# Kernel tuning notes

Measured on AMD Instinct MI355X. Metric: run time of the kernel, lower is better.

The kernel has to match this reference:

```python
import jax, jax.numpy as jnp
import numpy as np

H = 64; V = 50000; W = 64; N_TD = 8192; L_BU = 4096; N_BU = 2 * L_BU - 1; DEG = 2; NCLASS = 4


def setup_inputs() -> dict:
    rng = np.random.default_rng(0)
    def mat(*s):
        return jnp.asarray(rng.normal(scale=0.1, size=s).astype(np.float32))
    inp = {}
    inp['td_x_word'] = jnp.asarray(rng.random((N_TD, W), dtype=np.float32))
    inp['bu_x_word'] = jnp.asarray(rng.random((N_BU, W), dtype=np.float32))
    for tag in ('td', 'bu'):
        inp['E_' + tag] = mat(H, V)
        for g in ('z', 'r', 'h'):
            inp['W_%s_%s' % (g, tag)] = mat(H, H)
            inp['U_%s_%s' % (g, tag)] = mat(H, H)
            inp['b_%s_%s' % (g, tag)] = jnp.zeros((H,), jnp.float32)
    inp['W_out1'] = mat(H, 2 * H); inp['b_out1'] = jnp.zeros((H,), jnp.float32)
    inp['W_out4'] = mat(NCLASS, H); inp['b_out4'] = jnp.zeros((NCLASS,), jnp.float32)
    inp['td_x_index'] = jnp.asarray(rng.integers(0, V, (N_TD, W)).astype(np.int32))
    inp['bu_x_index'] = jnp.asarray(rng.integers(0, V, (N_BU, W)).astype(np.int32))
    # top-down: node i (stored at node_h row i+1) has parent at node_h row i//2 (row 0 = zero root)
    inp['td_parent'] = jnp.asarray((np.arange(N_TD) // 2).astype(np.int32))
    # leaves = node_h rows never used as a parent: rows (N_TD-1)//2+1 .. N_TD
    inp['td_leaf_idxs'] = jnp.asarray(np.arange((N_TD - 1) // 2 + 1, N_TD + 1).astype(np.int32))
    # bottom-up complete binary tree: leaves 0..L-1, parent j (node L+j) has children 2j, 2j+1
    tree = np.full((L_BU - 1, DEG + 1), -1, np.int32)
    j = np.arange(L_BU - 1)
    tree[:, 0] = 2 * j; tree[:, 1] = 2 * j + 1
    inp['bu_tree'] = jnp.asarray(tree)
    return inp


def _xe(E, idx, word):
    # E:[H,V], idx/word:[N,W] -> per-node embedding [N,H]
    return jnp.einsum('nwh,nw->nh', E.T[idx], word)


def _gru(zx, rx, hx, Uz, Ur, Uh, hprev):
    z = jax.nn.sigmoid(zx + Uz @ hprev)
    r = jax.nn.sigmoid(rx + Ur @ hprev)
    c = jnp.tanh(hx + Uh @ (hprev * r))
    return z * hprev + (1.0 - z) * c


def reference(td_x_word, bu_x_word, E_td, W_z_td, U_z_td, b_z_td, W_r_td, U_r_td, b_r_td,
              W_h_td, U_h_td, b_h_td, E_bu, W_z_bu, U_z_bu, b_z_bu, W_r_bu, U_r_bu, b_r_bu,
              W_h_bu, U_h_bu, b_h_bu, W_out1, b_out1, W_out4, b_out4,
              td_x_index, td_parent, td_leaf_idxs, bu_x_index, bu_tree):
    # ---- top-down tree GRU ----
    xe = _xe(E_td, td_x_index, td_x_word)                    # [N_td, H]
    zx = xe @ W_z_td.T + b_z_td
    rx = xe @ W_r_td.T + b_r_td
    hx = xe @ W_h_td.T + b_h_td
    n, h = xe.shape

    def td_step(node_h, i):
        hnew = _gru(zx[i], rx[i], hx[i], U_z_td, U_r_td, U_h_td, node_h[td_parent[i]])
        return node_h.at[i + 1].set(hnew), None

    node_h, _ = jax.lax.scan(td_step, jnp.zeros((n + 1, h), xe.dtype), jnp.arange(n))
    td_final = node_h[td_leaf_idxs].max(axis=0)              # [H]

    # ---- bottom-up tree GRU ----
    xe_b = _xe(E_bu, bu_x_index, bu_x_word)                  # [N_bu, H]
    zxb = xe_b @ W_z_bu.T + b_z_bu
    rxb = xe_b @ W_r_bu.T + b_r_bu
    hxb = xe_b @ W_h_bu.T + b_h_bu
    n_par = bu_tree.shape[0]
    n_b = xe_b.shape[0]
    L = n_b - n_par
    # leaves: child states are zeros => h_tilde = 0, r irrelevant, h = (1-z)*tanh(hx)
    leaf_h = (1.0 - jax.nn.sigmoid(zxb[:L])) * jnp.tanh(hxb[:L])
    node_hb0 = jnp.zeros((n_b, h), xe_b.dtype).at[:L].set(leaf_h)

    def bu_step(nh, j):
        idx = bu_tree[j, :-1]
        m = (idx > -1).astype(nh.dtype)
        h_tilde = (nh[jnp.clip(idx, 0)] * m[:, None]).sum(axis=0)
        hp = _gru(zxb[L + j], rxb[L + j], hxb[L + j], U_z_bu, U_r_bu, U_h_bu, h_tilde)
        return nh.at[L + j].set(hp), None

    node_hb, _ = jax.lax.scan(bu_step, node_hb0, jnp.arange(n_par))
    bu_root = node_hb[-1]                                    # [H]

    # ---- output head (forward() semantics: ReLU + softmax) ----
    fs = jnp.concatenate([td_final, bu_root])                # [2H]
    fs1 = jax.nn.relu(W_out1 @ fs + b_out1)                  # [H]
    return jax.nn.softmax(W_out4 @ fs1 + b_out4)             # [Nclass]
```

## Files before the change

kernel.cpp:

```cpp
#include <hip/hip_runtime.h>
#include <stdint.h>

typedef unsigned short u16;

#define V 50000
#define NTD 8192
#define NBU 8191

#define ET_TD_OFF   0ul
#define ET_BU_OFF   6400000ul
#define ZRH_TD_OFF  12800000ul
#define ZRH_BU_OFF  19091456ul
#define HBLEAF_OFF  25382144ul
#define TDMAX_OFF   26430720ul
#define BU6_OFF     26447104ul
#define BUROOT_OFF  26463488ul
#define CNT_OFF     26463744ul
#define WS_NEEDED   26464000ul

struct RvParams {
  const void *td_x_word, *bu_x_word;
  const int *td_idx, *bu_idx;
  const void *Wtd[3], *Utd[3], *btd[3];
  const void *Wbu[3], *Ubu[3], *bbu[3];
  const void *W_out1, *b_out1, *W_out4, *b_out4;
  const void *E_td, *E_bu;
  u16 *Et_td, *Et_bu;
  float *zrh_td, *zrh_bu, *hb_leaf, *tdmax, *bu6, *buroot;
  unsigned *cnt;
  void *out;
};

__device__ __forceinline__ float b2f(unsigned u){ return __uint_as_float(u << 16); }
__device__ __forceinline__ u16 f2b(float f){
  unsigned x = __float_as_uint(f);
  unsigned r = x + 0x7fffu + ((x >> 16) & 1u);
  return (u16)(r >> 16);
}
__device__ __forceinline__ float ldq(const void* p, bool f32, size_t i){
  return f32 ? ((const float*)p)[i] : b2f((unsigned)((const u16*)p)[i]);
}
__device__ __forceinline__ float sigm(float x){
  x = fminf(fmaxf(x, -30.f), 30.f);
  return 1.f / (1.f + __expf(-x));
}
__device__ __forceinline__ float tanh_f(float x){
  x = fminf(fmaxf(x, -15.f), 15.f);
  float e = __expf(2.f * x);
  return (e - 1.f) / (e + 1.f);
}
__device__ __forceinline__ float rdlane(float v, int k){
  return __uint_as_float((unsigned)__builtin_amdgcn_readlane((int)__float_as_uint(v), k));
}

__device__ __forceinline__ bool detect_f32_wave(const void* tdw, int lane){
  unsigned u = (unsigned)((const u16*)tdw)[lane];
  unsigned e = (u >> 7) & 0xFFu;
  int bad = ((u >> 15) | (e >= 0x7Fu ? 1u : 0u)) ? 1 : 0;
  unsigned long long m = __ballot(bad);
  return __popcll(m) >= 8;
}

__global__ __launch_bounds__(1024) void k0_transpose(RvParams p){
  const int tx = threadIdx.x & 63, ty = threadIdx.x >> 6;
  const bool f32 = detect_f32_wave(p.td_x_word, tx);
  if (blockIdx.x == 0 && threadIdx.x == 0){ p.cnt[0] = 0u; p.cnt[1] = 0u; }
  __shared__ u16 tile[64][66];
  const int nb = (V + 63) >> 6;
  int b = blockIdx.x;
  const void* src; u16* dst;
  if (b < nb){ src = p.E_td; dst = p.Et_td; }
  else       { src = p.E_bu; dst = p.Et_bu; b -= nb; }
  const int v0 = b << 6;
  #pragma unroll
  for (int i = 0; i < 4; i++){
    int h = ty + (i << 4);
    int v = v0 + tx;
    u16 val = 0;
    if (v < V){
      if (f32) val = f2b(((const float*)src)[(size_t)h * V + v]);
      else     val = ((const u16*)src)[(size_t)h * V + v];
    }
    tile[h][tx] = val;
  }
  __syncthreads();
  #pragma unroll
  for (int i = 0; i < 4; i++){
    int vv = ty + (i << 4);
    int v = v0 + vv;
    if (v < V) dst[(size_t)v * 64 + tx] = tile[tx][vv];
  }
}

__global__ __launch_bounds__(512) void k1_embed(RvParams p){
  const int tid = threadIdx.x, wv = tid >> 6, lane = tid & 63;
  const bool f32 = detect_f32_wave(p.td_x_word, lane);
  __shared__ float sWz[64 * 65], sWr[64 * 65], sWh[64 * 65];
  const bool is_td = blockIdx.x < 1024;
  {
    const void* Wzg = is_td ? p.Wtd[0] : p.Wbu[0];
    const void* Wrg = is_td ? p.Wtd[1] : p.Wbu[1];
    const void* Whg = is_td ? p.Wtd[2] : p.Wbu[2];
    #pragma unroll
    for (int q = 0; q < 8; q++){
      int u = tid + (q << 9);
      int i = u >> 6, k = u & 63;
      sWz[k * 65 + i] = ldq(Wzg, f32, u);
      sWr[k * 65 + i] = ldq(Wrg, f32, u);
      sWh[k * 65 + i] = ldq(Whg, f32, u);
    }
  }
  __syncthreads();
  const int gw = blockIdx.x * 8 + wv;
  int n; const void* xw; const int* xi; const u16* Et;
  if (is_td){ n = gw;        xw = p.td_x_word; xi = p.td_idx; Et = p.Et_td; }
  else      { n = gw - NTD;  xw = p.bu_x_word; xi = p.bu_idx; Et = p.Et_bu; }
  if (!is_td && n >= NBU) return;

  const int   my_idx = xi[(size_t)n * 64 + lane];
  const float my_w   = ldq(xw, f32, (size_t)n * 64 + lane);
  float x0 = 0.f, x1 = 0.f, x2 = 0.f, x3 = 0.f;
  #pragma unroll
  for (int w = 0; w < 64; w += 4){
    int   i0 = __builtin_amdgcn_readlane(my_idx, w);
    int   i1 = __builtin_amdgcn_readlane(my_idx, w + 1);
    int   i2 = __builtin_amdgcn_readlane(my_idx, w + 2);
    int   i3 = __builtin_amdgcn_readlane(my_idx, w + 3);
    x0 = fmaf(rdlane(my_w, w),     b2f((unsigned)Et[(size_t)i0 * 64 + lane]), x0);
    x1 = fmaf(rdlane(my_w, w + 1), b2f((unsigned)Et[(size_t)i1 * 64 + lane]), x1);
    x2 = fmaf(rdlane(my_w, w + 2), b2f((unsigned)Et[(size_t)i2 * 64 + lane]), x2);
    x3 = fmaf(rdlane(my_w, w + 3), b2f((unsigned)Et[(size_t)i3 * 64 + lane]), x3);
  }
  float xe = (x0 + x1) + (x2 + x3);

  float az = ldq(is_td ? p.btd[0] : p.bbu[0], f32, lane);
  float ar = ldq(is_td ? p.btd[1] : p.bbu[1], f32, lane);
  float ah = ldq(is_td ? p.btd[2] : p.bbu[2], f32, lane);
  #pragma unroll
  for (int k = 0; k < 64; k++){
    float xk = rdlane(xe, k);
    az = fmaf(sWz[k * 65 + lane], xk, az);
    ar = fmaf(sWr[k * 65 + lane], xk, ar);
    ah = fmaf(sWh[k * 65 + lane], xk, ah);
  }
  if (is_td){
    float* o = p.zrh_td + (size_t)n * 192;
    o[lane] = az; o[64 + lane] = ar; o[128 + lane] = ah;
  } else if (n < 4096){
    p.hb_leaf[(size_t)n * 64 + lane] = (1.f - sigm(az)) * tanh_f(ah);
  } else {
    float* o = p.zrh_bu + (size_t)n * 192;
    o[lane] = az; o[64 + lane] = ar; o[128 + lane] = ah;
  }
}

template<int NB>
__device__ __forceinline__ void gru_reg(const float (&uz)[64], const float (&ur)[64], const float (&uh)[64],
                                        float (&hp)[NB], const float (&zx)[NB], const float (&rx)[NB],
                                        const float (&hx)[NB], int lane){
  float az[NB], az2[NB], ar[NB], ar2[NB];
  #pragma unroll
  for (int n = 0; n < NB; n++){ az[n] = 0.f; az2[n] = 0.f; ar[n] = 0.f; ar2[n] = 0.f; }
  #pragma unroll
  for (int k = 0; k < 64; k += 2){
    #pragma unroll
    for (int n = 0; n < NB; n++){
      float h0 = rdlane(hp[n], k), h1 = rdlane(hp[n], k + 1);
      az[n]  = fmaf(uz[k],     h0, az[n]);
      az2[n] = fmaf(uz[k + 1], h1, az2[n]);
      ar[n]  = fmaf(ur[k],     h0, ar[n]);
      ar2[n] = fmaf(ur[k + 1], h1, ar2[n]);
    }
  }
  float z[NB], rh[NB];
  #pragma unroll
  for (int n = 0; n < NB; n++){
    z[n]  = sigm(zx[n] + az[n] + az2[n]);
    rh[n] = sigm(rx[n] + ar[n] + ar2[n]) * hp[n];
  }
  float ah[NB], ah2[NB];
  #pragma unroll
  for (int n = 0; n < NB; n++){ ah[n] = 0.f; ah2[n] = 0.f; }
  #pragma unroll
  for (int k = 0; k < 64; k += 2){
    #pragma unroll
    for (int n = 0; n < NB; n++){
      float r0 = rdlane(rh[n], k), r1 = rdlane(rh[n], k + 1);
      ah[n]  = fmaf(uh[k],     r0, ah[n]);
      ah2[n] = fmaf(uh[k + 1], r1, ah2[n]);
    }
  }
  #pragma unroll
  for (int n = 0; n < NB; n++){
    float c = tanh_f(hx[n] + ah[n] + ah2[n]);
    hp[n] = z[n] * hp[n] + (1.f - z[n]) * c;
  }
}

__device__ __forceinline__ void run_level(bool isbu, int cnt, int pbase, int base, int zoff,
                                          const float (&uz)[64], const float (&ur)[64], const float (&uh)[64],
                                          float* hbuf, const float* zbuf, int wv, int lane){
  if (cnt >= 16){
    for (int t0 = wv * 4; t0 < cnt; t0 += 16){
      float hp[4], zx[4], rx[4], hx[4];
      #pragma unroll
      for (int n = 0; n < 4; n++){
        int t = t0 + n;
        hp[n] = isbu ? (hbuf[(pbase + 2 * t) * 64 + lane] + hbuf[(pbase + 2 * t + 1) * 64 + lane])
                     : hbuf[(pbase + (t >> 1)) * 64 + lane];
        const float* zr = zbuf + (size_t)(base + zoff + t) * 192;
        zx[n] = zr[lane]; rx[n] = zr[64 + lane]; hx[n] = zr[128 + lane];
      }
      gru_reg<4>(uz, ur, uh, hp, zx, rx, hx, lane);
      #pragma unroll
      for (int n = 0; n < 4; n++) hbuf[(base + t0 + n) * 64 + lane] = hp[n];
    }
  } else {
    for (int t = wv; t < cnt; t += 4){
      float hp[1], zx[1], rx[1], hx[1];
      hp[0] = isbu ? (hbuf[(pbase + 2 * t) * 64 + lane] + hbuf[(pbase + 2 * t + 1) * 64 + lane])
                   : hbuf[(pbase + (t >> 1)) * 64 + lane];
      const float* zr = zbuf + (size_t)(base + zoff + t) * 192;
      zx[0] = zr[lane]; rx[0] = zr[64 + lane]; hx[0] = zr[128 + lane];
      gru_reg<1>(uz, ur, uh, hp, zx, rx, hx, lane);
      hbuf[(base + t) * 64 + lane] = hp[0];
    }
  }
  __syncthreads();
}

__global__ __launch_bounds__(256, 1) void k2_trees(RvParams p){
  const int tid = threadIdx.x, wv = tid >> 6, lane = tid & 63;
  const bool f32 = detect_f32_wave(p.td_x_word, lane);
  __shared__ __attribute__((aligned(16))) float zbuf[127 * 192];
  __shared__ __attribute__((aligned(16))) float hbuf[127 * 64];
  __shared__ __attribute__((aligned(16))) float scr[4 * 64];
  __shared__ int lastBU, lastAll;
  const bool is_td = blockIdx.x < 64;
  const int  b  = blockIdx.x;
  const int  bb = blockIdx.x - 64;

  float rzv[6], rrv[6], rhv[6], ezv[2], erv[2], ehv[2];
  if (is_td && wv == 0){
    int anc[7]; anc[6] = 63 + b;
    #pragma unroll
    for (int l = 5; l >= 1; l--) anc[l] = (anc[l + 1] - 1) >> 1;
    #pragma unroll
    for (int l = 1; l <= 6; l++){
      const float* zr = p.zrh_td + (size_t)(anc[l] - 1) * 192;
      rzv[l - 1] = zr[lane]; rrv[l - 1] = zr[64 + lane]; rhv[l - 1] = zr[128 + lane];
    }
    if (b == 0){
      #pragma unroll
      for (int n = 0; n < 2; n++){
        const float* zr = p.zrh_td + (size_t)(8190 + n) * 192;
        ezv[n] = zr[lane]; erv[n] = zr[64 + lane]; ehv[n] = zr[128 + lane];
      }
    }
  }

  if (is_td){
    for (int d = 1; d <= 6; d++){
      int cntn = 1 << d;
      size_t pos0 = ((size_t)(64 + b) << d) - 1;
      const float4* g = (const float4*)(p.zrh_td + (pos0 - 1) * 192);
      float4* s = (float4*)(zbuf + (size_t)(cntn - 1) * 192);
      int n4 = cntn * 48;
      for (int i = tid; i < n4; i += 256) s[i] = g[i];
    }
  } else {
    {
      const float4* g = (const float4*)(p.hb_leaf + (size_t)bb * 64 * 64);
      float4* s = (float4*)hbuf;
      for (int i = tid; i < 1024; i += 256) s[i] = g[i];
    }
    for (int l = 1; l <= 6; l++){
      int cntn = 1 << (6 - l);
      int baseC = 128 - (1 << (7 - l));
      {
        int j0 = 4096 - (1 << (13 - l)) + bb * cntn;
        const float4* g = (const float4*)(p.zrh_bu + (size_t)(4096 + j0) * 192);
        float4* s = (float4*)(zbuf + (size_t)baseC * 192);
        int n4 = cntn * 48;
        for (int i = tid; i < n4; i += 256) s[i] = g[i];
      }
      {
        int j0 = 4096 - (1 << (7 - l));
        const float4* g = (const float4*)(p.zrh_bu + (size_t)(4096 + j0) * 192);
        float4* s = (float4*)(zbuf + (size_t)(baseC - 64) * 192);
        int n4 = cntn * 48;
        for (int i = tid; i < n4; i += 256) s[i] = g[i];
      }
    }
  }

  float uz[64], ur[64], uh[64];
  {
    const void* Uzg = is_td ? p.Utd[0] : p.Ubu[0];
    const void* Urg = is_td ? p.Utd[1] : p.Ubu[1];
    const void* Uhg = is_td ? p.Utd[2] : p.Ubu[2];
    if (f32){
      const float4* a = (const float4*)((const float*)Uzg + (size_t)lane * 64);
      const float4* c = (const float4*)((const float*)Urg + (size_t)lane * 64);
      const float4* d = (const float4*)((const float*)Uhg + (size_t)lane * 64);
      #pragma unroll
      for (int q = 0; q < 16; q++){
        float4 vz = a[q], vr = c[q], vh = d[q];
        uz[4*q] = vz.x; uz[4*q+1] = vz.y; uz[4*q+2] = vz.z; uz[4*q+3] = vz.w;
        ur[4*q] = vr.x; ur[4*q+1] = vr.y; ur[4*q+2] = vr.z; ur[4*q+3] = vr.w;
        uh[4*q] = vh.x; uh[4*q+1] = vh.y; uh[4*q+2] = vh.z; uh[4*q+3] = vh.w;
      }
    } else {
      const u16* a = (const u16*)Uzg + (size_t)lane * 64;
      const u16* c = (const u16*)Urg + (size_t)lane * 64;
      const u16* d = (const u16*)Uhg + (size_t)lane * 64;
      #pragma unroll
      for (int k = 0; k < 64; k++){
        uz[k] = b2f((unsigned)a[k]); ur[k] = b2f((unsigned)c[k]); uh[k] = b2f((unsigned)d[k]);
      }
    }
  }
  __syncthreads();

  if (is_td){
    if (wv == 0){
      float hp[1] = {0.f}, zx[1], rx[1], hx[1];
      #pragma unroll
      for (int l = 0; l < 6; l++){
        zx[0] = rzv[l]; rx[0] = rrv[l]; hx[0] = rhv[l];
        gru_reg<1>(uz, ur, uh, hp, zx, rx, hx, lane);
      }
      hbuf[lane] = hp[0];
    }
    __syncthreads();
    for (int d = 1; d <= 6; d++)
      run_level(false, 1 << d, (1 << (d - 1)) - 1, (1 << d) - 1, 0, uz, ur, uh, hbuf, zbuf, wv, lane);
    if (b == 0 && wv == 0){
      float h4095 = hbuf[63 * 64 + lane];
      #pragma unroll
      for (int n = 0; n < 2; n++){
        float hp[1], zx[1], rx[1], hx[1];
        hp[0] = h4095; zx[0] = ezv[n]; rx[0] = erv[n]; hx[0] = ehv[n];
        gru_reg<1>(uz, ur, uh, hp, zx, rx, hx, lane);
        hbuf[(1 + n) * 64 + lane] = hp[0];
      }
    }
    __syncthreads();
    int cl = (b == 0) ? 65 : 64;
    float m = -3.0e38f;
    for (int i = wv; i < cl; i += 4){
      int s;
      if (b == 0) s = (i < 63) ? (64 + i) : ((i == 63) ? 1 : 2);
      else        s = 63 + i;
      m = fmaxf(m, hbuf[s * 64 + lane]);
    }
    scr[wv * 64 + lane] = m;
    __syncthreads();
    if (wv == 0){
      float mm = m;
      #pragma unroll
      for (int w2 = 1; w2 < 4; w2++) mm = fmaxf(mm, scr[w2 * 64 + lane]);
      p.tdmax[b * 64 + lane] = mm;
    }
  } else {
    for (int l = 1; l <= 6; l++)
      run_level(true, 1 << (6 - l), 128 - (1 << (8 - l)), 128 - (1 << (7 - l)), 0, uz, ur, uh, hbuf, zbuf, wv, lane);
    if (wv == 0) p.bu6[bb * 64 + lane] = hbuf[126 * 64 + lane];
    __threadfence();
    if (tid == 0){
      unsigned old = atomicAdd(&p.cnt[0], 1u);
      lastBU = (old == 63u) ? 1 : 0;
    }
    __syncthreads();
    if (lastBU){
      __threadfence();
      {
        const float4* g = (const float4*)p.bu6;
        float4* s = (float4*)hbuf;
        for (int i = tid; i < 1024; i += 256) s[i] = g[i];
      }
      __syncthreads();
      for (int l = 1; l <= 6; l++)
        run_level(true, 1 << (6 - l), 128 - (1 << (8 - l)), 128 - (1 << (7 - l)), -64, uz, ur, uh, hbuf, zbuf, wv, lane);
      if (wv == 0) p.buroot[lane] = hbuf[126 * 64 + lane];
    }
  }

  __threadfence();
  if (tid == 0){
    unsigned old = atomicAdd(&p.cnt[1], 1u);
    lastAll = (old == 127u) ? 1 : 0;
  }
  __syncthreads();
  if (lastAll){
    __threadfence();
    if (wv == 0){
      float m = -3.0e38f;
      #pragma unroll
      for (int bq = 0; bq < 64; bq++) m = fmaxf(m, p.tdmax[bq * 64 + lane]);
      scr[lane] = m;
      scr[64 + lane] = p.buroot[lane];
      __builtin_amdgcn_wave_barrier();
      float a = ldq(p.b_out1, f32, lane);
      for (int j = 0; j < 128; j++) a = fmaf(ldq(p.W_out1, f32, (size_t)lane * 128 + j), scr[j], a);
      scr[128 + lane] = fmaxf(a, 0.f);
      __builtin_amdgcn_wave_barrier();
      if (lane < 4){
        float l = ldq(p.b_out4, f32, lane);
        for (int i = 0; i < 64; i++) l = fmaf(ldq(p.W_out4, f32, (size_t)lane * 64 + i), scr[128 + i], l);
        scr[192 + lane] = l;
      }
      __builtin_amdgcn_wave_barrier();
      if (lane < 4){
        float l0 = scr[192], l1 = scr[193], l2 = scr[194], l3 = scr[195];
        float mx = fmaxf(fmaxf(l0, l1), fmaxf(l2, l3));
        float s = __expf(l0 - mx) + __expf(l1 - mx) + __expf(l2 - mx) + __expf(l3 - mx);
        float prob = __expf(scr[192 + lane] - mx) / s;
        if (f32) ((float*)p.out)[lane] = prob;
        else     ((u16*)p.out)[lane]   = f2b(prob);
      }
    }
  }
}

extern "C" void kernel_launch(void* const* d_in, const int* in_sizes, int n_in,
                              void* d_out, int out_size, void* d_ws, size_t ws_size,
                              hipStream_t stream){
  if (ws_size < WS_NEEDED) return;
  RvParams p;
  p.td_x_word = d_in[0];
  p.bu_x_word = d_in[1];
  p.E_td = d_in[2];
  p.Wtd[0] = d_in[3];  p.Utd[0] = d_in[4];  p.btd[0] = d_in[5];
  p.Wtd[1] = d_in[6];  p.Utd[1] = d_in[7];  p.btd[1] = d_in[8];
  p.Wtd[2] = d_in[9];  p.Utd[2] = d_in[10]; p.btd[2] = d_in[11];
  p.E_bu = d_in[12];
  p.Wbu[0] = d_in[13]; p.Ubu[0] = d_in[14]; p.bbu[0] = d_in[15];
  p.Wbu[1] = d_in[16]; p.Ubu[1] = d_in[17]; p.bbu[1] = d_in[18];
  p.Wbu[2] = d_in[19]; p.Ubu[2] = d_in[20]; p.bbu[2] = d_in[21];
  p.W_out1 = d_in[22]; p.b_out1 = d_in[23];
  p.W_out4 = d_in[24]; p.b_out4 = d_in[25];
  p.td_idx = (const int*)d_in[26];
  const bool dict_order = (in_sizes[27] == NBU * 64);
  p.bu_idx = (const int*)d_in[dict_order ? 27 : 29];

  char* w = (char*)d_ws;
  p.Et_td  = (u16*)  (w + ET_TD_OFF);
  p.Et_bu  = (u16*)  (w + ET_BU_OFF);
  p.zrh_td = (float*)(w + ZRH_TD_OFF);
  p.zrh_bu = (float*)(w + ZRH_BU_OFF);
  p.hb_leaf= (float*)(w + HBLEAF_OFF);
  p.tdmax  = (float*)(w + TDMAX_OFF);
  p.bu6    = (float*)(w + BU6_OFF);
  p.buroot = (float*)(w + BUROOT_OFF);
  p.cnt    = (unsigned*)(w + CNT_OFF);
  p.out    = d_out;

  const int nb = (V + 63) / 64;
  k0_transpose<<<2 * nb, 1024, 0, stream>>>(p);
  k1_embed   <<<2048,    512,  0, stream>>>(p);
  k2_trees   <<<128,     256,  0, stream>>>(p);
}
```

Before: 245.9 us.

## Pack GRU weights as bf16 pairs in registers and restructure embed and tree kernels

Weight matrices are now staged through LDS as packed bf16 pairs and held in 32 registers per gate instead of 64 floats. The embed kernel processes four nodes per wave with register-resident weights across 512 blocks. The tree kernel moves to 512 threads, drops the large LDS zrh staging buffer in favour of per-wave register prefetch of gate inputs, and unrolls each tree level explicitly. The aim is to cut register pressure and LDS traffic, raise per-block parallelism and amortize weight loads. The trade-off is that f32 weights get rounded to bf16, which adds precision loss, and the embed gather now reads index and word values as scalar loads per node.

```diff
diff --git a/kernel.cpp b/kernel.cpp
--- a/kernel.cpp
+++ b/kernel.cpp
@@ -37,6 +37,8 @@
   unsigned r = x + 0x7fffu + ((x >> 16) & 1u);
   return (u16)(r >> 16);
 }
+__device__ __forceinline__ float pklo(unsigned u){ return __uint_as_float(u << 16); }
+__device__ __forceinline__ float pkhi(unsigned u){ return __uint_as_float(u & 0xffff0000u); }
 __device__ __forceinline__ float ldq(const void* p, bool f32, size_t i){
   return f32 ? ((const float*)p)[i] : b2f((unsigned)((const u16*)p)[i]);
 }
@@ -59,6 +61,30 @@
   int bad = ((u >> 15) | (e >= 0x7Fu ? 1u : 0u)) ? 1 : 0;
   unsigned long long m = __ballot(bad);
   return __popcll(m) >= 8;
+}
+
+template<int BT>
+__device__ __forceinline__ void stage_w_packed(unsigned* dst, const void* src, bool f32, int tid){
+  for (int u = tid; u < 2048; u += BT){
+    int q = u & 31, i = u >> 5;
+    unsigned pk;
+    if (f32){
+      float a = ((const float*)src)[i * 64 + 2 * q];
+      float b = ((const float*)src)[i * 64 + 2 * q + 1];
+      pk = (unsigned)f2b(a) | ((unsigned)f2b(b) << 16);
+    } else {
+      pk = ((const unsigned*)src)[i * 32 + q];
+    }
+    dst[q * 65 + i] = pk;
+  }
+}
+__device__ __forceinline__ void load_w_regs(unsigned (&w)[32], const unsigned* lds, int lane){
+  #pragma unroll
+  for (int q = 0; q < 32; q++) w[q] = lds[q * 65 + lane];
+}
+__device__ __forceinline__ void ld3(const float* zrh, size_t idx, float& a, float& b, float& c, int lane){
+  const float* zr = zrh + idx * 192;
+  a = zr[lane]; b = zr[64 + lane]; c = zr[128 + lane];
 }
 
 __global__ __launch_bounds__(1024) void k0_transpose(RvParams p){
@@ -92,84 +118,96 @@
   }
 }
 
-__global__ __launch_bounds__(512) void k1_embed(RvParams p){
+__global__ __launch_bounds__(512, 2) void k1_embed(RvParams p){
   const int tid = threadIdx.x, wv = tid >> 6, lane = tid & 63;
   const bool f32 = detect_f32_wave(p.td_x_word, lane);
-  __shared__ float sWz[64 * 65], sWr[64 * 65], sWh[64 * 65];
-  const bool is_td = blockIdx.x < 1024;
-  {
-    const void* Wzg = is_td ? p.Wtd[0] : p.Wbu[0];
-    const void* Wrg = is_td ? p.Wtd[1] : p.Wbu[1];
-    const void* Whg = is_td ? p.Wtd[2] : p.Wbu[2];
-    #pragma unroll
-    for (int q = 0; q < 8; q++){
-      int u = tid + (q << 9);
-      int i = u >> 6, k = u & 63;
-      sWz[k * 65 + i] = ldq(Wzg, f32, u);
-      sWr[k * 65 + i] = ldq(Wrg, f32, u);
-      sWh[k * 65 + i] = ldq(Whg, f32, u);
-    }
-  }
+  __shared__ unsigned sW0[32 * 65], sW1[32 * 65], sW2[32 * 65];
+  const bool is_td = blockIdx.x < 256;
+  stage_w_packed<512>(sW0, is_td ? p.Wtd[0] : p.Wbu[0], f32, tid);
+  stage_w_packed<512>(sW1, is_td ? p.Wtd[1] : p.Wbu[1], f32, tid);
+  stage_w_packed<512>(sW2, is_td ? p.Wtd[2] : p.Wbu[2], f32, tid);
   __syncthreads();
-  const int gw = blockIdx.x * 8 + wv;
-  int n; const void* xw; const int* xi; const u16* Et;
-  if (is_td){ n = gw;        xw = p.td_x_word; xi = p.td_idx; Et = p.Et_td; }
-  else      { n = gw - NTD;  xw = p.bu_x_word; xi = p.bu_idx; Et = p.Et_bu; }
-  if (!is_td && n >= NBU) return;
-
-  const int   my_idx = xi[(size_t)n * 64 + lane];
-  const float my_w   = ldq(xw, f32, (size_t)n * 64 + lane);
-  float x0 = 0.f, x1 = 0.f, x2 = 0.f, x3 = 0.f;
-  #pragma unroll
-  for (int w = 0; w < 64; w += 4){
-    int   i0 = __builtin_amdgcn_readlane(my_idx, w);
-    int   i1 = __builtin_amdgcn_readlane(my_idx, w + 1);
-    int   i2 = __builtin_amdgcn_readlane(my_idx, w + 2);
-    int   i3 = __builtin_amdgcn_readlane(my_idx, w + 3);
-    x0 = fmaf(rdlane(my_w, w),     b2f((unsigned)Et[(size_t)i0 * 64 + lane]), x0);
-    x1 = fmaf(rdlane(my_w, w + 1), b2f((unsigned)Et[(size_t)i1 * 64 + lane]), x1);
-    x2 = fmaf(rdlane(my_w, w + 2), b2f((unsigned)Et[(size_t)i2 * 64 + lane]), x2);
-    x3 = fmaf(rdlane(my_w, w + 3), b2f((unsigned)Et[(size_t)i3 * 64 + lane]), x3);
-  }
-  float xe = (x0 + x1) + (x2 + x3);
-
-  float az = ldq(is_td ? p.btd[0] : p.bbu[0], f32, lane);
-  float ar = ldq(is_td ? p.btd[1] : p.bbu[1], f32, lane);
-  float ah = ldq(is_td ? p.btd[2] : p.bbu[2], f32, lane);
-  #pragma unroll
-  for (int k = 0; k < 64; k++){
-    float xk = rdlane(xe, k);
-    az = fmaf(sWz[k * 65 + lane], xk, az);
-    ar = fmaf(sWr[k * 65 + lane], xk, ar);
-    ah = fmaf(sWh[k * 65 + lane], xk, ah);
-  }
-  if (is_td){
-    float* o = p.zrh_td + (size_t)n * 192;
-    o[lane] = az; o[64 + lane] = ar; o[128 + lane] = ah;
-  } else if (n < 4096){
-    p.hb_leaf[(size_t)n * 64 + lane] = (1.f - sigm(az)) * tanh_f(ah);
-  } else {
-    float* o = p.zrh_bu + (size_t)n * 192;
-    o[lane] = az; o[64 + lane] = ar; o[128 + lane] = ah;
+  unsigned wz[32], wr[32], wh[32];
+  load_w_regs(wz, sW0, lane);
+  load_w_regs(wr, sW1, lane);
+  load_w_regs(wh, sW2, lane);
+
+  const int fam  = is_td ? blockIdx.x : (blockIdx.x - 256);
+  const int n0   = fam * 32 + wv * 4;
+  const int nmax = is_td ? NTD : NBU;
+  const int*  xi = is_td ? p.td_idx : p.bu_idx;
+  const void* xw = is_td ? p.td_x_word : p.bu_x_word;
+  const u16*  Et = is_td ? p.Et_td : p.Et_bu;
+
+  int nn[4]; bool val[4];
+  #pragma unroll
+  for (int j = 0; j < 4; j++){
+    val[j] = (n0 + j < nmax);
+    nn[j]  = val[j] ? (n0 + j) : (nmax - 1);
+  }
+  float xe[4] = {0.f, 0.f, 0.f, 0.f};
+  #pragma unroll 8
+  for (int w = 0; w < 64; w++){
+    #pragma unroll
+    for (int j = 0; j < 4; j++){
+      int   iw = xi[(size_t)nn[j] * 64 + w];
+      float wd = ldq(xw, f32, (size_t)nn[j] * 64 + w);
+      xe[j] = fmaf(wd, b2f((unsigned)Et[(size_t)iw * 64 + lane]), xe[j]);
+    }
+  }
+  float az[4], az2[4], ar[4], ar2[4], ah[4], ah2[4];
+  #pragma unroll
+  for (int j = 0; j < 4; j++){ az[j]=az2[j]=ar[j]=ar2[j]=ah[j]=ah2[j]=0.f; }
+  #pragma unroll
+  for (int q = 0; q < 32; q++){
+    float z0 = pklo(wz[q]), z1 = pkhi(wz[q]);
+    float r0 = pklo(wr[q]), r1 = pkhi(wr[q]);
+    float g0 = pklo(wh[q]), g1 = pkhi(wh[q]);
+    #pragma unroll
+    for (int j = 0; j < 4; j++){
+      float x0 = rdlane(xe[j], 2 * q), x1 = rdlane(xe[j], 2 * q + 1);
+      az[j] = fmaf(z0, x0, az[j]);  az2[j] = fmaf(z1, x1, az2[j]);
+      ar[j] = fmaf(r0, x0, ar[j]);  ar2[j] = fmaf(r1, x1, ar2[j]);
+      ah[j] = fmaf(g0, x0, ah[j]);  ah2[j] = fmaf(g1, x1, ah2[j]);
+    }
+  }
+  float bz = ldq(is_td ? p.btd[0] : p.bbu[0], f32, lane);
+  float br = ldq(is_td ? p.btd[1] : p.bbu[1], f32, lane);
+  float bh = ldq(is_td ? p.btd[2] : p.bbu[2], f32, lane);
+  #pragma unroll
+  for (int j = 0; j < 4; j++){
+    if (!val[j]) continue;
+    int n = n0 + j;
+    float zxv = bz + az[j] + az2[j];
+    float rxv = br + ar[j] + ar2[j];
+    float hxv = bh + ah[j] + ah2[j];
+    if (is_td){
+      float* o = p.zrh_td + (size_t)n * 192;
+      o[lane] = zxv; o[64 + lane] = rxv; o[128 + lane] = hxv;
+    } else if (n < 4096){
+      p.hb_leaf[(size_t)n * 64 + lane] = (1.f - sigm(zxv)) * tanh_f(hxv);
+    } else {
+      float* o = p.zrh_bu + (size_t)n * 192;
+      o[lane] = zxv; o[64 + lane] = rxv; o[128 + lane] = hxv;
+    }
   }
 }
 
 template<int NB>
-__device__ __forceinline__ void gru_reg(const float (&uz)[64], const float (&ur)[64], const float (&uh)[64],
-                                        float (&hp)[NB], const float (&zx)[NB], const float (&rx)[NB],
-                                        const float (&hx)[NB], int lane){
+__device__ __forceinline__ void gru_pk(const unsigned (&uz)[32], const unsigned (&ur)[32], const unsigned (&uh)[32],
+                                       float (&hp)[NB], const float* zx, const float* rx, const float* hx){
   float az[NB], az2[NB], ar[NB], ar2[NB];
   #pragma unroll
-  for (int n = 0; n < NB; n++){ az[n] = 0.f; az2[n] = 0.f; ar[n] = 0.f; ar2[n] = 0.f; }
-  #pragma unroll
-  for (int k = 0; k < 64; k += 2){
+  for (int n = 0; n < NB; n++){ az[n] = az2[n] = ar[n] = ar2[n] = 0.f; }
+  #pragma unroll
+  for (int q = 0; q < 32; q++){
+    float wz0 = pklo(uz[q]), wz1 = pkhi(uz[q]);
+    float wr0 = pklo(ur[q]), wr1 = pkhi(ur[q]);
     #pragma unroll
     for (int n = 0; n < NB; n++){
-      float h0 = rdlane(hp[n], k), h1 = rdlane(hp[n], k + 1);
-      az[n]  = fmaf(uz[k],     h0, az[n]);
-      az2[n] = fmaf(uz[k + 1], h1, az2[n]);
-      ar[n]  = fmaf(ur[k],     h0, ar[n]);
-      ar2[n] = fmaf(ur[k + 1], h1, ar2[n]);
+      float h0 = rdlane(hp[n], 2 * q), h1 = rdlane(hp[n], 2 * q + 1);
+      az[n] = fmaf(wz0, h0, az[n]);  az2[n] = fmaf(wz1, h1, az2[n]);
+      ar[n] = fmaf(wr0, h0, ar[n]);  ar2[n] = fmaf(wr1, h1, ar2[n]);
     }
   }
   float z[NB], rh[NB];
@@ -180,14 +218,14 @@
   }
   float ah[NB], ah2[NB];
   #pragma unroll
-  for (int n = 0; n < NB; n++){ ah[n] = 0.f; ah2[n] = 0.f; }
-  #pragma unroll
-  for (int k = 0; k < 64; k += 2){
+  for (int n = 0; n < NB; n++){ ah[n] = ah2[n] = 0.f; }
+  #pragma unroll
+  for (int q = 0; q < 32; q++){
+    float wh0 = pklo(uh[q]), wh1 = pkhi(uh[q]);
     #pragma unroll
     for (int n = 0; n < NB; n++){
-      float r0 = rdlane(rh[n], k), r1 = rdlane(rh[n], k + 1);
-      ah[n]  = fmaf(uh[k],     r0, ah[n]);
-      ah2[n] = fmaf(uh[k + 1], r1, ah2[n]);
+      float r0 = rdlane(rh[n], 2 * q), r1 = rdlane(rh[n], 2 * q + 1);
+      ah[n] = fmaf(wh0, r0, ah[n]);  ah2[n] = fmaf(wh1, r1, ah2[n]);
     }
   }
   #pragma unroll
@@ -197,158 +235,131 @@
   }
 }
 
-__device__ __forceinline__ void run_level(bool isbu, int cnt, int pbase, int base, int zoff,
-                                          const float (&uz)[64], const float (&ur)[64], const float (&uh)[64],
-                                          float* hbuf, const float* zbuf, int wv, int lane){
-  if (cnt >= 16){
-    for (int t0 = wv * 4; t0 < cnt; t0 += 16){
-      float hp[4], zx[4], rx[4], hx[4];
-      #pragma unroll
-      for (int n = 0; n < 4; n++){
-        int t = t0 + n;
-        hp[n] = isbu ? (hbuf[(pbase + 2 * t) * 64 + lane] + hbuf[(pbase + 2 * t + 1) * 64 + lane])
-                     : hbuf[(pbase + (t >> 1)) * 64 + lane];
-        const float* zr = zbuf + (size_t)(base + zoff + t) * 192;
-        zx[n] = zr[lane]; rx[n] = zr[64 + lane]; hx[n] = zr[128 + lane];
-      }
-      gru_reg<4>(uz, ur, uh, hp, zx, rx, hx, lane);
-      #pragma unroll
-      for (int n = 0; n < 4; n++) hbuf[(base + t0 + n) * 64 + lane] = hp[n];
-    }
-  } else {
-    for (int t = wv; t < cnt; t += 4){
-      float hp[1], zx[1], rx[1], hx[1];
-      hp[0] = isbu ? (hbuf[(pbase + 2 * t) * 64 + lane] + hbuf[(pbase + 2 * t + 1) * 64 + lane])
-                   : hbuf[(pbase + (t >> 1)) * 64 + lane];
-      const float* zr = zbuf + (size_t)(base + zoff + t) * 192;
-      zx[0] = zr[lane]; rx[0] = zr[64 + lane]; hx[0] = zr[128 + lane];
-      gru_reg<1>(uz, ur, uh, hp, zx, rx, hx, lane);
-      hbuf[(base + t) * 64 + lane] = hp[0];
-    }
-  }
-  __syncthreads();
-}
-
-__global__ __launch_bounds__(256, 1) void k2_trees(RvParams p){
+template<int NB>
+__device__ __forceinline__ void td_nodes(const unsigned (&uz)[32], const unsigned (&ur)[32], const unsigned (&uh)[32],
+                                         float* hbuf, int pbase, int base, int t0,
+                                         const float* zx, const float* rx, const float* hx, int lane){
+  float hp[NB];
+  #pragma unroll
+  for (int n = 0; n < NB; n++) hp[n] = hbuf[(pbase + ((t0 + n) >> 1)) * 64 + lane];
+  gru_pk<NB>(uz, ur, uh, hp, zx, rx, hx);
+  #pragma unroll
+  for (int n = 0; n < NB; n++) hbuf[(base + t0 + n) * 64 + lane] = hp[n];
+}
+template<int NB>
+__device__ __forceinline__ void bu_nodes(const unsigned (&uz)[32], const unsigned (&ur)[32], const unsigned (&uh)[32],
+                                         float* hbuf, int baseP, int baseC, int t0,
+                                         const float* zx, const float* rx, const float* hx, int lane){
+  float hp[NB];
+  #pragma unroll
+  for (int n = 0; n < NB; n++){
+    int t = t0 + n;
+    hp[n] = hbuf[(baseP + 2 * t) * 64 + lane] + hbuf[(baseP + 2 * t + 1) * 64 + lane];
+  }
+  gru_pk<NB>(uz, ur, uh, hp, zx, rx, hx);
+  #pragma unroll
+  for (int n = 0; n < NB; n++) hbuf[(baseC + t0 + n) * 64 + lane] = hp[n];
+}
+
+__global__ __launch_bounds__(512, 2) void k2_trees(RvParams p){
   const int tid = threadIdx.x, wv = tid >> 6, lane = tid & 63;
   const bool f32 = detect_f32_wave(p.td_x_word, lane);
-  __shared__ __attribute__((aligned(16))) float zbuf[127 * 192];
   __shared__ __attribute__((aligned(16))) float hbuf[127 * 64];
-  __shared__ __attribute__((aligned(16))) float scr[4 * 64];
+  __shared__ unsigned sU0[32 * 65], sU1[32 * 65], sU2[32 * 65];
+  __shared__ float scr[8 * 64];
   __shared__ int lastBU, lastAll;
   const bool is_td = blockIdx.x < 64;
   const int  b  = blockIdx.x;
   const int  bb = blockIdx.x - 64;
 
+  float pz[10], pr[10], ph[10];
   float rzv[6], rrv[6], rhv[6], ezv[2], erv[2], ehv[2];
-  if (is_td && wv == 0){
-    int anc[7]; anc[6] = 63 + b;
-    #pragma unroll
-    for (int l = 5; l >= 1; l--) anc[l] = (anc[l + 1] - 1) >> 1;
-    #pragma unroll
-    for (int l = 1; l <= 6; l++){
-      const float* zr = p.zrh_td + (size_t)(anc[l] - 1) * 192;
-      rzv[l - 1] = zr[lane]; rrv[l - 1] = zr[64 + lane]; rhv[l - 1] = zr[128 + lane];
-    }
-    if (b == 0){
-      #pragma unroll
-      for (int n = 0; n < 2; n++){
-        const float* zr = p.zrh_td + (size_t)(8190 + n) * 192;
-        ezv[n] = zr[lane]; erv[n] = zr[64 + lane]; ehv[n] = zr[128 + lane];
-      }
-    }
-  }
-
   if (is_td){
-    for (int d = 1; d <= 6; d++){
-      int cntn = 1 << d;
-      size_t pos0 = ((size_t)(64 + b) << d) - 1;
-      const float4* g = (const float4*)(p.zrh_td + (pos0 - 1) * 192);
-      float4* s = (float4*)(zbuf + (size_t)(cntn - 1) * 192);
-      int n4 = cntn * 48;
-      for (int i = tid; i < n4; i += 256) s[i] = g[i];
+    const size_t B = (size_t)(64 + b);
+    if (wv < 2) ld3(p.zrh_td, (B << 1) - 2 + wv, pz[0], pr[0], ph[0], lane);
+    if (wv < 4) ld3(p.zrh_td, (B << 2) - 2 + wv, pz[1], pr[1], ph[1], lane);
+    ld3(p.zrh_td, (B << 3) - 2 + wv, pz[2], pr[2], ph[2], lane);
+    #pragma unroll
+    for (int n = 0; n < 2; n++) ld3(p.zrh_td, (B << 4) - 2 + wv * 2 + n, pz[3 + n], pr[3 + n], ph[3 + n], lane);
+    #pragma unroll
+    for (int n = 0; n < 4; n++) ld3(p.zrh_td, (B << 5) - 2 + wv * 4 + n, pz[5 + n], pr[5 + n], ph[5 + n], lane);
+    if (wv == 0){
+      int anc[7]; anc[6] = 63 + b;
+      #pragma unroll
+      for (int l = 5; l >= 1; l--) anc[l] = (anc[l + 1] - 1) >> 1;
+      #pragma unroll
+      for (int l = 1; l <= 6; l++) ld3(p.zrh_td, (size_t)(anc[l] - 1), rzv[l - 1], rrv[l - 1], rhv[l - 1], lane);
+      if (b == 0){
+        #pragma unroll
+        for (int n = 0; n < 2; n++) ld3(p.zrh_td, (size_t)(8190 + n), ezv[n], erv[n], ehv[n], lane);
+      }
     }
   } else {
+    #pragma unroll
+    for (int n = 0; n < 4; n++) ld3(p.zrh_bu, (size_t)4096 + bb * 32 + wv * 4 + n, pz[n], pr[n], ph[n], lane);
+    #pragma unroll
+    for (int n = 0; n < 2; n++) ld3(p.zrh_bu, (size_t)4096 + 2048 + bb * 16 + wv * 2 + n, pz[4 + n], pr[4 + n], ph[4 + n], lane);
+    ld3(p.zrh_bu, (size_t)4096 + 3072 + bb * 8 + wv, pz[6], pr[6], ph[6], lane);
+    if (wv < 4) ld3(p.zrh_bu, (size_t)4096 + 3584 + bb * 4 + wv, pz[7], pr[7], ph[7], lane);
+    if (wv < 2) ld3(p.zrh_bu, (size_t)4096 + 3840 + bb * 2 + wv, pz[8], pr[8], ph[8], lane);
+    if (wv == 0) ld3(p.zrh_bu, (size_t)4096 + 3968 + bb, pz[9], pr[9], ph[9], lane);
     {
       const float4* g = (const float4*)(p.hb_leaf + (size_t)bb * 64 * 64);
       float4* s = (float4*)hbuf;
-      for (int i = tid; i < 1024; i += 256) s[i] = g[i];
-    }
-    for (int l = 1; l <= 6; l++){
-      int cntn = 1 << (6 - l);
-      int baseC = 128 - (1 << (7 - l));
-      {
-        int j0 = 4096 - (1 << (13 - l)) + bb * cntn;
-        const float4* g = (const float4*)(p.zrh_bu + (size_t)(4096 + j0) * 192);
-        float4* s = (float4*)(zbuf + (size_t)baseC * 192);
-        int n4 = cntn * 48;
-        for (int i = tid; i < n4; i += 256) s[i] = g[i];
-      }
-      {
-        int j0 = 4096 - (1 << (7 - l));
-        const float4* g = (const float4*)(p.zrh_bu + (size_t)(4096 + j0) * 192);
-        float4* s = (float4*)(zbuf + (size_t)(baseC - 64) * 192);
-        int n4 = cntn * 48;
-        for (int i = tid; i < n4; i += 256) s[i] = g[i];
-      }
-    }
-  }
-
-  float uz[64], ur[64], uh[64];
-  {
-    const void* Uzg = is_td ? p.Utd[0] : p.Ubu[0];
-    const void* Urg = is_td ? p.Utd[1] : p.Ubu[1];
-    const void* Uhg = is_td ? p.Utd[2] : p.Ubu[2];
-    if (f32){
-      const float4* a = (const float4*)((const float*)Uzg + (size_t)lane * 64);
-      const float4* c = (const float4*)((const float*)Urg + (size_t)lane * 64);
-      const float4* d = (const float4*)((const float*)Uhg + (size_t)lane * 64);
-      #pragma unroll
-      for (int q = 0; q < 16; q++){
-        float4 vz = a[q], vr = c[q], vh = d[q];
-        uz[4*q] = vz.x; uz[4*q+1] = vz.y; uz[4*q+2] = vz.z; uz[4*q+3] = vz.w;
-        ur[4*q] = vr.x; ur[4*q+1] = vr.y; ur[4*q+2] = vr.z; ur[4*q+3] = vr.w;
-        uh[4*q] = vh.x; uh[4*q+1] = vh.y; uh[4*q+2] = vh.z; uh[4*q+3] = vh.w;
-      }
-    } else {
-      const u16* a = (const u16*)Uzg + (size_t)lane * 64;
-      const u16* c = (const u16*)Urg + (size_t)lane * 64;
-      const u16* d = (const u16*)Uhg + (size_t)lane * 64;
-      #pragma unroll
-      for (int k = 0; k < 64; k++){
-        uz[k] = b2f((unsigned)a[k]); ur[k] = b2f((unsigned)c[k]); uh[k] = b2f((unsigned)d[k]);
-      }
-    }
-  }
+      for (int i = tid; i < 1024; i += 512) s[i] = g[i];
+    }
+  }
+  stage_w_packed<512>(sU0, is_td ? p.Utd[0] : p.Ubu[0], f32, tid);
+  stage_w_packed<512>(sU1, is_td ? p.Utd[1] : p.Ubu[1], f32, tid);
+  stage_w_packed<512>(sU2, is_td ? p.Utd[2] : p.Ubu[2], f32, tid);
   __syncthreads();
+  unsigned uz[32], ur[32], uh[32];
+  load_w_regs(uz, sU0, lane);
+  load_w_regs(ur, sU1, lane);
+  load_w_regs(uh, sU2, lane);
 
   if (is_td){
     if (wv == 0){
-      float hp[1] = {0.f}, zx[1], rx[1], hx[1];
-      #pragma unroll
-      for (int l = 0; l < 6; l++){
-        zx[0] = rzv[l]; rx[0] = rrv[l]; hx[0] = rhv[l];
-        gru_reg<1>(uz, ur, uh, hp, zx, rx, hx, lane);
-      }
+      float hp[1] = {0.f};
+      #pragma unroll
+      for (int l = 0; l < 6; l++) gru_pk<1>(uz, ur, uh, hp, &rzv[l], &rrv[l], &rhv[l]);
       hbuf[lane] = hp[0];
     }
     __syncthreads();
-    for (int d = 1; d <= 6; d++)
-      run_level(false, 1 << d, (1 << (d - 1)) - 1, (1 << d) - 1, 0, uz, ur, uh, hbuf, zbuf, wv, lane);
+    if (wv < 2) td_nodes<1>(uz, ur, uh, hbuf, 0, 1, wv, &pz[0], &pr[0], &ph[0], lane);
+    __syncthreads();
+    if (wv < 4) td_nodes<1>(uz, ur, uh, hbuf, 1, 3, wv, &pz[1], &pr[1], &ph[1], lane);
+    __syncthreads();
+    td_nodes<1>(uz, ur, uh, hbuf, 3, 7, wv, &pz[2], &pr[2], &ph[2], lane);
+    __syncthreads();
+    td_nodes<2>(uz, ur, uh, hbuf, 7, 15, wv * 2, &pz[3], &pr[3], &ph[3], lane);
+    __syncthreads();
+    td_nodes<4>(uz, ur, uh, hbuf, 15, 31, wv * 4, &pz[5], &pr[5], &ph[5], lane);
+    __syncthreads();
+    {
+      float za[4], ra[4], ha[4], zb[4], rb[4], hb2[4];
+      const size_t B = (size_t)(64 + b);
+      #pragma unroll
+      for (int n = 0; n < 4; n++) ld3(p.zrh_td, (B << 6) - 2 + wv * 4 + n, za[n], ra[n], ha[n], lane);
+      #pragma unroll
+      for (int n = 0; n < 4; n++) ld3(p.zrh_td, (B << 6) - 2 + 32 + wv * 4 + n, zb[n], rb[n], hb2[n], lane);
+      td_nodes<4>(uz, ur, uh, hbuf, 31, 63, wv * 4, za, ra, ha, lane);
+      td_nodes<4>(uz, ur, uh, hbuf, 31, 63, 32 + wv * 4, zb, rb, hb2, lane);
+    }
+    __syncthreads();
     if (b == 0 && wv == 0){
       float h4095 = hbuf[63 * 64 + lane];
       #pragma unroll
       for (int n = 0; n < 2; n++){
-        float hp[1], zx[1], rx[1], hx[1];
-        hp[0] = h4095; zx[0] = ezv[n]; rx[0] = erv[n]; hx[0] = ehv[n];
-        gru_reg<1>(uz, ur, uh, hp, zx, rx, hx, lane);
+        float hp[1] = {h4095};
+        gru_pk<1>(uz, ur, uh, hp, &ezv[n], &erv[n], &ehv[n]);
         hbuf[(1 + n) * 64 + lane] = hp[0];
       }
     }
     __syncthreads();
     int cl = (b == 0) ? 65 : 64;
     float m = -3.0e38f;
-    for (int i = wv; i < cl; i += 4){
+    for (int i = wv; i < cl; i += 8){
       int s;
       if (b == 0) s = (i < 63) ? (64 + i) : ((i == 63) ? 1 : 2);
       else        s = 63 + i;
@@ -359,12 +370,23 @@
     if (wv == 0){
       float mm = m;
       #pragma unroll
-      for (int w2 = 1; w2 < 4; w2++) mm = fmaxf(mm, scr[w2 * 64 + lane]);
+      for (int w2 = 1; w2 < 8; w2++) mm = fmaxf(mm, scr[w2 * 64 + lane]);
       p.tdmax[b * 64 + lane] = mm;
     }
   } else {
-    for (int l = 1; l <= 6; l++)
-      run_level(true, 1 << (6 - l), 128 - (1 << (8 - l)), 128 - (1 << (7 - l)), 0, uz, ur, uh, hbuf, zbuf, wv, lane);
+    __syncthreads();
+    bu_nodes<4>(uz, ur, uh, hbuf, 0, 64, wv * 4, &pz[0], &pr[0], &ph[0], lane);
+    __syncthreads();
+    bu_nodes<2>(uz, ur, uh, hbuf, 64, 96, wv * 2, &pz[4], &pr[4], &ph[4], lane);
+    __syncthreads();
+    bu_nodes<1>(uz, ur, uh, hbuf, 96, 112, wv, &pz[6], &pr[6], &ph[6], lane);
+    __syncthreads();
+    if (wv < 4) bu_nodes<1>(uz, ur, uh, hbuf, 112, 120, wv, &pz[7], &pr[7], &ph[7], lane);
+    __syncthreads();
+    if (wv < 2) bu_nodes<1>(uz, ur, uh, hbuf, 120, 124, wv, &pz[8], &pr[8], &ph[8], lane);
+    __syncthreads();
+    if (wv == 0) bu_nodes<1>(uz, ur, uh, hbuf, 124, 126, 0, &pz[9], &pr[9], &ph[9], lane);
+    __syncthreads();
     if (wv == 0) p.bu6[bb * 64 + lane] = hbuf[126 * 64 + lane];
     __threadfence();
     if (tid == 0){
@@ -374,15 +396,37 @@
     __syncthreads();
     if (lastBU){
       __threadfence();
-      {
-        const float4* g = (const float4*)p.bu6;
+      { const float4* g = (const float4*)p.bu6;
         float4* s = (float4*)hbuf;
-        for (int i = tid; i < 1024; i += 256) s[i] = g[i];
-      }
+        for (int i = tid; i < 1024; i += 512) s[i] = g[i]; }
       __syncthreads();
-      for (int l = 1; l <= 6; l++)
-        run_level(true, 1 << (6 - l), 128 - (1 << (8 - l)), 128 - (1 << (7 - l)), -64, uz, ur, uh, hbuf, zbuf, wv, lane);
-      if (wv == 0) p.buroot[lane] = hbuf[126 * 64 + lane];
+      float tz[4], tr2[4], th[4];
+      #pragma unroll
+      for (int n = 0; n < 4; n++) ld3(p.zrh_bu, (size_t)8128 + wv * 4 + n, tz[n], tr2[n], th[n], lane);
+      bu_nodes<4>(uz, ur, uh, hbuf, 0, 64, wv * 4, tz, tr2, th, lane);
+      __syncthreads();
+      #pragma unroll
+      for (int n = 0; n < 2; n++) ld3(p.zrh_bu, (size_t)8160 + wv * 2 + n, tz[n], tr2[n], th[n], lane);
+      bu_nodes<2>(uz, ur, uh, hbuf, 64, 96, wv * 2, tz, tr2, th, lane);
+      __syncthreads();
+      ld3(p.zrh_bu, (size_t)8176 + wv, tz[0], tr2[0], th[0], lane);
+      bu_nodes<1>(uz, ur, uh, hbuf, 96, 112, wv, tz, tr2, th, lane);
+      __syncthreads();
+      if (wv < 4){
+        ld3(p.zrh_bu, (size_t)8184 + wv, tz[0], tr2[0], th[0], lane);
+        bu_nodes<1>(uz, ur, uh, hbuf, 112, 120, wv, tz, tr2, th, lane);
+      }
+      __syncthreads();
+      if (wv < 2){
+        ld3(p.zrh_bu, (size_t)8188 + wv, tz[0], tr2[0], th[0], lane);
+        bu_nodes<1>(uz, ur, uh, hbuf, 120, 124, wv, tz, tr2, th, lane);
+      }
+      __syncthreads();
+      if (wv == 0){
+        ld3(p.zrh_bu, (size_t)8190, tz[0], tr2[0], th[0], lane);
+        bu_nodes<1>(uz, ur, uh, hbuf, 124, 126, 0, tz, tr2, th, lane);
+        p.buroot[lane] = hbuf[126 * 64 + lane];
+      }
     }
   }
 
@@ -458,6 +502,6 @@
 
   const int nb = (V + 63) / 64;
   k0_transpose<<<2 * nb, 1024, 0, stream>>>(p);
-  k1_embed   <<<2048,    512,  0, stream>>>(p);
-  k2_trees   <<<128,     256,  0, stream>>>(p);
-}
+  k1_embed   <<<512,     512,  0, stream>>>(p);
+  k2_trees   <<<128,     512,  0, stream>>>(p);
+}
```

Result: slower. 423.8 us (+72.4%).

## Vectorize embedding gather with 16-byte row loads and bf16-packed register weights

Applied to the files above, without the earlier changes.

The embedding gather now has each lane load 16 bytes (8 bf16 values) of an embedding row, with 8 lanes per row, so one wave covers 8 words per step instead of issuing 64 scalar 2-byte loads. Partial sums are then reduced across lane groups with xor shuffles. The W projection weights are packed as bf16 pairs in LDS and then held in registers, which removes per-k LDS reads in the projection loop. Launch bounds now request 2 blocks per SM. The costs are higher register pressure, extra shuffle work for the reduction, and bf16 rounding of W even when the inputs are f32.

```diff
diff --git a/kernel.cpp b/kernel.cpp
--- a/kernel.cpp
+++ b/kernel.cpp
@@ -37,6 +37,8 @@
   unsigned r = x + 0x7fffu + ((x >> 16) & 1u);
   return (u16)(r >> 16);
 }
+__device__ __forceinline__ float pklo(unsigned u){ return __uint_as_float(u << 16); }
+__device__ __forceinline__ float pkhi(unsigned u){ return __uint_as_float(u & 0xffff0000u); }
 __device__ __forceinline__ float ldq(const void* p, bool f32, size_t i){
   return f32 ? ((const float*)p)[i] : b2f((unsigned)((const u16*)p)[i]);
 }
@@ -59,6 +61,26 @@
   int bad = ((u >> 15) | (e >= 0x7Fu ? 1u : 0u)) ? 1 : 0;
   unsigned long long m = __ballot(bad);
   return __popcll(m) >= 8;
+}
+
+template<int BT>
+__device__ __forceinline__ void stage_w_packed(unsigned* dst, const void* src, bool f32, int tid){
+  for (int u = tid; u < 2048; u += BT){
+    int q = u & 31, i = u >> 5;
+    unsigned pk;
+    if (f32){
+      float a = ((const float*)src)[i * 64 + 2 * q];
+      float b = ((const float*)src)[i * 64 + 2 * q + 1];
+      pk = (unsigned)f2b(a) | ((unsigned)f2b(b) << 16);
+    } else {
+      pk = ((const unsigned*)src)[i * 32 + q];
+    }
+    dst[q * 65 + i] = pk;
+  }
+}
+__device__ __forceinline__ void load_w_regs(unsigned (&w)[32], const unsigned* lds, int lane){
+  #pragma unroll
+  for (int q = 0; q < 32; q++) w[q] = lds[q * 65 + lane];
 }
 
 __global__ __launch_bounds__(1024) void k0_transpose(RvParams p){
@@ -92,25 +114,20 @@
   }
 }
 
-__global__ __launch_bounds__(512) void k1_embed(RvParams p){
+__global__ __launch_bounds__(512, 2) void k1_embed(RvParams p){
   const int tid = threadIdx.x, wv = tid >> 6, lane = tid & 63;
   const bool f32 = detect_f32_wave(p.td_x_word, lane);
-  __shared__ float sWz[64 * 65], sWr[64 * 65], sWh[64 * 65];
+  __shared__ unsigned sW0[32 * 65], sW1[32 * 65], sW2[32 * 65];
   const bool is_td = blockIdx.x < 1024;
-  {
-    const void* Wzg = is_td ? p.Wtd[0] : p.Wbu[0];
-    const void* Wrg = is_td ? p.Wtd[1] : p.Wbu[1];
-    const void* Whg = is_td ? p.Wtd[2] : p.Wbu[2];
-    #pragma unroll
-    for (int q = 0; q < 8; q++){
-      int u = tid + (q << 9);
-      int i = u >> 6, k = u & 63;
-      sWz[k * 65 + i] = ldq(Wzg, f32, u);
-      sWr[k * 65 + i] = ldq(Wrg, f32, u);
-      sWh[k * 65 + i] = ldq(Whg, f32, u);
-    }
-  }
+  stage_w_packed<512>(sW0, is_td ? p.Wtd[0] : p.Wbu[0], f32, tid);
+  stage_w_packed<512>(sW1, is_td ? p.Wtd[1] : p.Wbu[1], f32, tid);
+  stage_w_packed<512>(sW2, is_td ? p.Wtd[2] : p.Wbu[2], f32, tid);
   __syncthreads();
+  unsigned wz[32], wr[32], wh[32];
+  load_w_regs(wz, sW0, lane);
+  load_w_regs(wr, sW1, lane);
+  load_w_regs(wh, sW2, lane);
+
   const int gw = blockIdx.x * 8 + wv;
   int n; const void* xw; const int* xi; const u16* Et;
   if (is_td){ n = gw;        xw = p.td_x_word; xi = p.td_idx; Et = p.Et_td; }
@@ -119,38 +136,55 @@
 
   const int   my_idx = xi[(size_t)n * 64 + lane];
   const float my_w   = ldq(xw, f32, (size_t)n * 64 + lane);
-  float x0 = 0.f, x1 = 0.f, x2 = 0.f, x3 = 0.f;
-  #pragma unroll
-  for (int w = 0; w < 64; w += 4){
-    int   i0 = __builtin_amdgcn_readlane(my_idx, w);
-    int   i1 = __builtin_amdgcn_readlane(my_idx, w + 1);
-    int   i2 = __builtin_amdgcn_readlane(my_idx, w + 2);
-    int   i3 = __builtin_amdgcn_readlane(my_idx, w + 3);
-    x0 = fmaf(rdlane(my_w, w),     b2f((unsigned)Et[(size_t)i0 * 64 + lane]), x0);
-    x1 = fmaf(rdlane(my_w, w + 1), b2f((unsigned)Et[(size_t)i1 * 64 + lane]), x1);
-    x2 = fmaf(rdlane(my_w, w + 2), b2f((unsigned)Et[(size_t)i2 * 64 + lane]), x2);
-    x3 = fmaf(rdlane(my_w, w + 3), b2f((unsigned)Et[(size_t)i3 * 64 + lane]), x3);
-  }
-  float xe = (x0 + x1) + (x2 + x3);
-
-  float az = ldq(is_td ? p.btd[0] : p.bbu[0], f32, lane);
-  float ar = ldq(is_td ? p.btd[1] : p.bbu[1], f32, lane);
-  float ah = ldq(is_td ? p.btd[2] : p.bbu[2], f32, lane);
-  #pragma unroll
-  for (int k = 0; k < 64; k++){
-    float xk = rdlane(xe, k);
-    az = fmaf(sWz[k * 65 + lane], xk, az);
-    ar = fmaf(sWr[k * 65 + lane], xk, ar);
-    ah = fmaf(sWh[k * 65 + lane], xk, ah);
-  }
+  const int g = lane >> 3, s = lane & 7;
+
+  float acc[8];
+  #pragma unroll
+  for (int j = 0; j < 8; j++) acc[j] = 0.f;
+  #pragma unroll
+  for (int t = 0; t < 8; t++){
+    int   srcl = 8 * t + g;
+    int   idxr = __shfl(my_idx, srcl);
+    float wd   = __shfl(my_w, srcl);
+    const uint4 row = *(const uint4*)((const char*)Et + (((size_t)(unsigned)idxr) << 7) + (s << 4));
+    acc[0] = fmaf(wd, pklo(row.x), acc[0]);
+    acc[1] = fmaf(wd, pkhi(row.x), acc[1]);
+    acc[2] = fmaf(wd, pklo(row.y), acc[2]);
+    acc[3] = fmaf(wd, pkhi(row.y), acc[3]);
+    acc[4] = fmaf(wd, pklo(row.z), acc[4]);
+    acc[5] = fmaf(wd, pkhi(row.z), acc[5]);
+    acc[6] = fmaf(wd, pklo(row.w), acc[6]);
+    acc[7] = fmaf(wd, pkhi(row.w), acc[7]);
+  }
+  #pragma unroll
+  for (int j = 0; j < 8; j++){
+    acc[j] += __shfl_xor(acc[j], 8);
+    acc[j] += __shfl_xor(acc[j], 16);
+    acc[j] += __shfl_xor(acc[j], 32);
+  }
+  float az = 0.f, az2 = 0.f, ar = 0.f, ar2 = 0.f, ah = 0.f, ah2 = 0.f;
+  #pragma unroll
+  for (int q = 0; q < 32; q++){
+    float x0 = rdlane(acc[(2 * q) & 7],     (2 * q) >> 3);
+    float x1 = rdlane(acc[(2 * q + 1) & 7], (2 * q + 1) >> 3);
+    az  = fmaf(pklo(wz[q]), x0, az);   az2 = fmaf(pkhi(wz[q]), x1, az2);
+    ar  = fmaf(pklo(wr[q]), x0, ar);   ar2 = fmaf(pkhi(wr[q]), x1, ar2);
+    ah  = fmaf(pklo(wh[q]), x0, ah);   ah2 = fmaf(pkhi(wh[q]), x1, ah2);
+  }
+  float bz = ldq(is_td ? p.btd[0] : p.bbu[0], f32, lane);
+  float br = ldq(is_td ? p.btd[1] : p.bbu[1], f32, lane);
+  float bh = ldq(is_td ? p.btd[2] : p.bbu[2], f32, lane);
+  float zxv = bz + az + az2;
+  float rxv = br + ar + ar2;
+  float hxv = bh + ah + ah2;
   if (is_td){
     float* o = p.zrh_td + (size_t)n * 192;
-    o[lane] = az; o[64 + lane] = ar; o[128 + lane] = ah;
+    o[lane] = zxv; o[64 + lane] = rxv; o[128 + lane] = hxv;
   } else if (n < 4096){
-    p.hb_leaf[(size_t)n * 64 + lane] = (1.f - sigm(az)) * tanh_f(ah);
+    p.hb_leaf[(size_t)n * 64 + lane] = (1.f - sigm(zxv)) * tanh_f(hxv);
   } else {
     float* o = p.zrh_bu + (size_t)n * 192;
-    o[lane] = az; o[64 + lane] = ar; o[128 + lane] = ah;
+    o[lane] = zxv; o[64 + lane] = rxv; o[128 + lane] = hxv;
   }
 }
 
@@ -374,11 +408,9 @@
     __syncthreads();
     if (lastBU){
       __threadfence();
-      {
-        const float4* g = (const float4*)p.bu6;
+      { const float4* g = (const float4*)p.bu6;
         float4* s = (float4*)hbuf;
-        for (int i = tid; i < 1024; i += 256) s[i] = g[i];
-      }
+        for (int i = tid; i < 1024; i += 256) s[i] = g[i]; }
       __syncthreads();
       for (int l = 1; l <= 6; l++)
         run_level(true, 1 << (6 - l), 128 - (1 << (8 - l)), 128 - (1 << (7 - l)), -64, uz, ur, uh, hbuf, zbuf, wv, lane);
```

Result: slower. 251.9 us (+2.5%).
